# Kernel tuning notes

Measured on AMD Instinct MI355X. Metric: run time of the kernel, lower is better.

## Reference

```python
import jax, jax.numpy as jnp
import numpy as np

N_NODES = 100000
N_EDGES = 1600000
C_IN, C_HID, C_OUT = 32, 32, 8
N_AGENTS = 1000


def _glorot(key, shape):
    fan_in, fan_out = shape[0], shape[1]
    lim = float(np.sqrt(6.0 / (fan_in + fan_out)))
    return jax.random.uniform(key, shape, jnp.float32, -lim, lim)


def setup_inputs() -> dict:
    key = jax.random.key(0)
    ks = jax.random.split(key, 16)
    x = jax.random.normal(ks[0], (N_NODES, C_IN), jnp.float32)
    edge_index = jax.random.randint(ks[1], (2, N_EDGES), 0, N_NODES, jnp.int64)
    d = {"x": x, "edge_index": edge_index}
    dims = [(C_IN, C_HID), (C_HID, C_HID), (C_HID, C_HID)]
    for i, (di, do) in enumerate(dims, start=1):
        d[f"W_l{i}"] = _glorot(ks[2 * i], (di, do))        # neighbor (aggregated) weight
        d[f"b_l{i}"] = jnp.zeros((do,), jnp.float32)
        d[f"W_r{i}"] = _glorot(ks[2 * i + 1], (di, do))    # root/self weight (no bias)
    d["W_out"] = _glorot(ks[10], (C_HID, C_OUT))
    d["b_out"] = jnp.zeros((C_OUT,), jnp.float32)
    return d


def _sage_conv(x, src, dst, W_l, b_l, W_r):
    # mean-aggregate neighbor features at destination nodes
    msg = x[src]                                               # [E, d] gather
    summed = jax.ops.segment_sum(msg, dst, num_segments=N_NODES)
    cnt = jax.ops.segment_sum(jnp.ones((src.shape[0],), x.dtype), dst,
                              num_segments=N_NODES)
    agg = summed / jnp.maximum(cnt, 1.0)[:, None]              # deg==0 -> 0
    return agg @ W_l + b_l + x @ W_r


def reference(x, edge_index, W_l1, b_l1, W_r1, W_l2, b_l2, W_r2,
              W_l3, b_l3, W_r3, W_out, b_out):
    src, dst = edge_index[0], edge_index[1]
    h = jax.nn.relu(_sage_conv(x, src, dst, W_l1, b_l1, W_r1))
    h = jax.nn.relu(_sage_conv(h, src, dst, W_l2, b_l2, W_r2))
    h = jax.nn.relu(_sage_conv(h, src, dst, W_l3, b_l3, W_r3))
    out = h @ W_out + b_out
    return out[:N_AGENTS]
```

## Files before the change

### kernel.cpp

```cpp
#include <hip/hip_runtime.h>
#include <hip/hip_bf16.h>

#define N_NODES 100000
#define N_EDGES 1600000
#define N_AGENTS 1000

#define NB 782
#define ABLK 512
#define CHUNK (N_EDGES / ABLK)
#define CONV_BLOCKS 3125
#define FLAGS_I4 25024
#define FLAG_BLOCKS 98

typedef short s16x8 __attribute__((ext_vector_type(8)));
typedef float f32x4 __attribute__((ext_vector_type(4)));

__device__ __forceinline__ unsigned short f2bf(float f) {
    unsigned u = __float_as_uint(f);
    u += 0x7fffu + ((u >> 16) & 1u);
    return (unsigned short)(u >> 16);
}
__device__ __forceinline__ float bflo(unsigned u) { return __uint_as_float(u << 16); }
__device__ __forceinline__ float bfhi(unsigned u) { return __uint_as_float(u & 0xffff0000u); }

__global__ __launch_bounds__(256) void hist_prep_kernel(
    const int* __restrict__ dst, int* __restrict__ partialT,
    const float* __restrict__ x, unsigned short* __restrict__ xb,
    const float* __restrict__ Wl1, const float* __restrict__ Wr1,
    const float* __restrict__ Wl2, const float* __restrict__ Wr2,
    const float* __restrict__ Wl3, const float* __restrict__ Wr3,
    unsigned short* __restrict__ Wcat, int* __restrict__ flags)
{
    int b = blockIdx.x;
    if (b < ABLK) {
        __shared__ int hist[NB];
        for (int i = threadIdx.x; i < NB; i += 256) hist[i] = 0;
        __syncthreads();
        int beg = b * CHUNK;
        for (int e = beg + threadIdx.x; e < beg + CHUNK; e += 256)
            atomicAdd(&hist[dst[e] >> 7], 1);
        __syncthreads();
        for (int i = threadIdx.x; i < NB; i += 256) partialT[i * ABLK + b] = hist[i];
    } else if (b < ABLK + CONV_BLOCKS) {
        int i = (b - ABLK) * 256 + threadIdx.x;
        float4 v = ((const float4*)x)[i];
        ((ushort4*)xb)[i] = make_ushort4(f2bf(v.x), f2bf(v.y), f2bf(v.z), f2bf(v.w));
    } else if (b < ABLK + CONV_BLOCKS + 24) {
        int gid = (b - ABLK - CONV_BLOCKS) * 256 + threadIdx.x;
        int L = gid >> 11, idx = gid & 2047;
        int k = idx >> 5, n = idx & 31;
        const float* Wl = (L == 0) ? Wl1 : (L == 1) ? Wl2 : Wl3;
        const float* Wr = (L == 0) ? Wr1 : (L == 1) ? Wr2 : Wr3;
        float v = (k < 32) ? Wl[k * 32 + n] : Wr[(k - 32) * 32 + n];
        Wcat[gid] = f2bf(v);
    } else {
        int gid = (b - ABLK - CONV_BLOCKS - 24) * 256 + threadIdx.x;
        if (gid < FLAGS_I4) ((int4*)flags)[gid] = make_int4(0, 0, 0, 0);
    }
}

__global__ __launch_bounds__(256) void bucket_prefix_kernel(
    const int* __restrict__ partialT, int* __restrict__ baseT, int* __restrict__ tot)
{
    int wave = threadIdx.x >> 6, lane = threadIdx.x & 63;
    int t = blockIdx.x * 4 + wave;
    if (t >= NB) return;
    const int4* p = (const int4*)(partialT + (size_t)t * ABLK);
    int4 u0 = p[lane * 2], u1 = p[lane * 2 + 1];
    int v0 = u0.x, v1 = u0.y, v2 = u0.z, v3 = u0.w;
    int v4 = u1.x, v5 = u1.y, v6 = u1.z, v7 = u1.w;
    int p0 = 0, p1 = v0, p2 = p1 + v1, p3 = p2 + v2;
    int p4 = p3 + v3, p5 = p4 + v4, p6 = p5 + v5, p7 = p6 + v6;
    int s = p7 + v7;
    int x = s;
    #pragma unroll
    for (int off = 1; off < 64; off <<= 1) {
        int y = __shfl_up(x, off);
        if (lane >= off) x += y;
    }
    int excl = x - s;
    int4* q = (int4*)(baseT + (size_t)t * ABLK);
    q[lane * 2]     = make_int4(excl + p0, excl + p1, excl + p2, excl + p3);
    q[lane * 2 + 1] = make_int4(excl + p4, excl + p5, excl + p6, excl + p7);
    if (lane == 63) tot[t] = x;
}

__global__ __launch_bounds__(256) void bucket_scatter_kernel(
    const int* __restrict__ src, const int* __restrict__ dst,
    const int* __restrict__ baseT, const int* __restrict__ tot,
    int* __restrict__ bstart, int* __restrict__ ebuf)
{
    __shared__ int cur[NB];
    __shared__ int tsum[256];
    int b = blockIdx.x, t = threadIdx.x;
    int i0 = t * 4;
    int v0 = (i0     < NB) ? tot[i0]     : 0;
    int v1 = (i0 + 1 < NB) ? tot[i0 + 1] : 0;
    int v2 = (i0 + 2 < NB) ? tot[i0 + 2] : 0;
    int v3 = (i0 + 3 < NB) ? tot[i0 + 3] : 0;
    int p1 = v0, p2 = v0 + v1, p3 = v0 + v1 + v2, s4 = p3 + v3;
    tsum[t] = s4;
    __syncthreads();
    for (int off = 1; off < 256; off <<= 1) {
        int u = (t >= off) ? tsum[t - off] : 0;
        __syncthreads();
        tsum[t] += u;
        __syncthreads();
    }
    int excl = tsum[t] - s4;
    int st0 = excl, st1 = excl + p1, st2 = excl + p2, st3 = excl + p3;
    if (i0     < NB) cur[i0]     = st0 + baseT[(size_t)i0 * ABLK + b];
    if (i0 + 1 < NB) cur[i0 + 1] = st1 + baseT[(size_t)(i0 + 1) * ABLK + b];
    if (i0 + 2 < NB) cur[i0 + 2] = st2 + baseT[(size_t)(i0 + 2) * ABLK + b];
    if (i0 + 3 < NB) cur[i0 + 3] = st3 + baseT[(size_t)(i0 + 3) * ABLK + b];
    if (b == 0) {
        if (i0     < NB) bstart[i0]     = st0;
        if (i0 + 1 < NB) bstart[i0 + 1] = st1;
        if (i0 + 2 < NB) bstart[i0 + 2] = st2;
        if (i0 + 3 < NB) bstart[i0 + 3] = st3;
        if (t == 255)    bstart[NB] = tsum[255];
    }
    __syncthreads();
    int beg = b * CHUNK;
    for (int e = beg + threadIdx.x; e < beg + CHUNK; e += 256) {
        int d = dst[e];
        int slot = atomicAdd(&cur[d >> 7], 1);
        ebuf[slot] = src[e] | ((d & 127) << 17);
    }
}

__global__ __launch_bounds__(256) void bucket_csr_kernel(
    const int* __restrict__ bstart, const int* __restrict__ ebuf,
    int* __restrict__ rowptr, float* __restrict__ inv, int* __restrict__ esrc,
    int* __restrict__ flags)
{
    __shared__ int hist4[512], cur4[512], tmp[256];
    int b = blockIdx.x;
    int t = threadIdx.x;
    int beg = bstart[b], end = bstart[b + 1];
    hist4[t] = 0; hist4[t + 256] = 0;
    __syncthreads();
    for (int i = beg + t; i < end; i += 256) {
        int p = ebuf[i];
        int ln = (p >> 17) & 127;
        int cls = (p & 0x1FFFF) >> 15;
        atomicAdd(&hist4[ln * 4 + cls], 1);
    }
    __syncthreads();
    int c0 = 0, c1 = 0, c2 = 0, c3 = 0, v = 0;
    if (t < 128) {
        c0 = hist4[t * 4 + 0]; c1 = hist4[t * 4 + 1];
        c2 = hist4[t * 4 + 2]; c3 = hist4[t * 4 + 3];
        v = c0 + c1 + c2 + c3;
    }
    tmp[t] = v;
    __syncthreads();
    for (int off = 1; off < 256; off <<= 1) {
        int u = (t >= off) ? tmp[t - off] : 0;
        __syncthreads();
        tmp[t] += u;
        __syncthreads();
    }
    int excl = tmp[t] - v;
    int node = b * 128 + t;
    if (t < 128 && node < N_NODES) {
        int start = beg + excl;
        rowptr[node] = start;
        inv[node] = 1.0f / fmaxf((float)v, 1.0f);
        cur4[t * 4 + 0] = start;
        cur4[t * 4 + 1] = start + c0;
        cur4[t * 4 + 2] = start + c0 + c1;
        cur4[t * 4 + 3] = start + c0 + c1 + c2;
        if (node < N_AGENTS) flags[node] = 1;
    }
    if (b == NB - 1 && t == 0) rowptr[N_NODES] = N_EDGES;
    __syncthreads();
    bool agent_bucket = (b < 8);
    for (int i = beg + t; i < end; i += 256) {
        int p = ebuf[i];
        int ln = (p >> 17) & 127;
        int s = p & 0x1FFFF;
        int slot = atomicAdd(&cur4[ln * 4 + (s >> 15)], 1);
        esrc[slot] = s;
        if (agent_bucket && (b * 128 + ln) < N_AGENTS)
            flags[s] = 1;
    }
}

__global__ __launch_bounds__(256) void sage_fused_kernel(
    const int* __restrict__ rowptr, const int* __restrict__ esrc,
    const float* __restrict__ inv, const unsigned short* __restrict__ hb,
    const unsigned short* __restrict__ Wcat, const float* __restrict__ bl,
    const float* __restrict__ Wout, const float* __restrict__ bout,
    void* __restrict__ outp, int n_nodes, int final)
{
    __shared__ unsigned short sW[2048];
    __shared__ float sb[32];
    __shared__ unsigned short smean[64 * 40];
    __shared__ float sh3[64 * 33];
    __shared__ float sWo[256];
    __shared__ float sbo[8];

    int tid = threadIdx.x;
    ((uint4*)sW)[tid] = ((const uint4*)Wcat)[tid];
    if (tid < 32) sb[tid] = bl[tid];
    if (final) {
        sWo[tid] = Wout[tid];
        if (tid < 8) sbo[tid] = bout[tid];
    }

    int lane = tid & 63, wave = tid >> 6;

    int g = lane >> 2, q = lane & 3;
    int nodeA = blockIdx.x * 64 + wave * 16 + g;
    int beg = 0, end = 0;
    if (nodeA < n_nodes) { beg = rowptr[nodeA]; end = rowptr[nodeA + 1]; }
    float a0 = 0.f, a1 = 0.f, a2 = 0.f, a3 = 0.f;
    float a4 = 0.f, a5 = 0.f, a6 = 0.f, a7 = 0.f;
    int j = beg;
    for (; j + 3 < end; j += 4) {
        int s0 = esrc[j];
        int s1 = esrc[j + 1];
        int s2 = esrc[j + 2];
        int s3 = esrc[j + 3];
        uint4 u0 = *(const uint4*)(hb + s0 * 32 + q * 8);
        uint4 u1 = *(const uint4*)(hb + s1 * 32 + q * 8);
        uint4 u2 = *(const uint4*)(hb + s2 * 32 + q * 8);
        uint4 u3 = *(const uint4*)(hb + s3 * 32 + q * 8);
        a0 += bflo(u0.x); a1 += bfhi(u0.x);
        a2 += bflo(u0.y); a3 += bfhi(u0.y);
        a4 += bflo(u0.z); a5 += bfhi(u0.z);
        a6 += bflo(u0.w); a7 += bfhi(u0.w);
        a0 += bflo(u1.x); a1 += bfhi(u1.x);
        a2 += bflo(u1.y); a3 += bfhi(u1.y);
        a4 += bflo(u1.z); a5 += bfhi(u1.z);
        a6 += bflo(u1.w); a7 += bfhi(u1.w);
        a0 += bflo(u2.x); a1 += bfhi(u2.x);
        a2 += bflo(u2.y); a3 += bfhi(u2.y);
        a4 += bflo(u2.z); a5 += bfhi(u2.z);
        a6 += bflo(u2.w); a7 += bfhi(u2.w);
        a0 += bflo(u3.x); a1 += bfhi(u3.x);
        a2 += bflo(u3.y); a3 += bfhi(u3.y);
        a4 += bflo(u3.z); a5 += bfhi(u3.z);
        a6 += bflo(u3.w); a7 += bfhi(u3.w);
    }
    for (; j < end; j++) {
        int s = esrc[j];
        uint4 u = *(const uint4*)(hb + s * 32 + q * 8);
        a0 += bflo(u.x); a1 += bfhi(u.x);
        a2 += bflo(u.y); a3 += bfhi(u.y);
        a4 += bflo(u.z); a5 += bfhi(u.z);
        a6 += bflo(u.w); a7 += bfhi(u.w);
    }
    float iv = (nodeA < n_nodes) ? inv[nodeA] : 0.f;
    uint4 o;
    o.x = (unsigned)f2bf(a0 * iv) | ((unsigned)f2bf(a1 * iv) << 16);
    o.y = (unsigned)f2bf(a2 * iv) | ((unsigned)f2bf(a3 * iv) << 16);
    o.z = (unsigned)f2bf(a4 * iv) | ((unsigned)f2bf(a5 * iv) << 16);
    o.w = (unsigned)f2bf(a6 * iv) | ((unsigned)f2bf(a7 * iv) << 16);
    int mrow = wave * 16 + g;
    *(uint4*)&smean[mrow * 40 + q * 8] = o;
    __syncthreads();

    int l15 = lane & 15, quad = lane >> 4;
    s16x8 bf_[2][2];
    #pragma unroll
    for (int kt = 0; kt < 2; kt++)
        #pragma unroll
        for (int nt = 0; nt < 2; nt++)
            #pragma unroll
            for (int jj = 0; jj < 8; jj++) {
                int k = kt * 32 + quad * 8 + jj;
                bf_[kt][nt][jj] = (short)sW[k * 32 + l15 + nt * 16];
            }
    float bias0 = sb[l15], bias1 = sb[l15 + 16];

    int tilebase = blockIdx.x * 64 + wave * 16;
    int nodeD = tilebase + l15;
    int na = min(nodeD, n_nodes - 1);
    s16x8 am = *(const s16x8*)&smean[(wave * 16 + l15) * 40 + quad * 8];
    s16x8 as = *(const s16x8*)(hb + (size_t)na * 32 + quad * 8);
    f32x4 acc0 = {0.f, 0.f, 0.f, 0.f};
    f32x4 acc1 = {0.f, 0.f, 0.f, 0.f};
    acc0 = __builtin_amdgcn_mfma_f32_16x16x32_bf16(am, bf_[0][0], acc0, 0, 0, 0);
    acc0 = __builtin_amdgcn_mfma_f32_16x16x32_bf16(as, bf_[1][0], acc0, 0, 0, 0);
    acc1 = __builtin_amdgcn_mfma_f32_16x16x32_bf16(am, bf_[0][1], acc1, 0, 0, 0);
    acc1 = __builtin_amdgcn_mfma_f32_16x16x32_bf16(as, bf_[1][1], acc1, 0, 0, 0);

    if (!final) {
        #pragma unroll
        for (int r = 0; r < 4; r++) {
            int onode = tilebase + quad * 4 + r;
            if (onode < n_nodes) {
                ((unsigned short*)outp)[onode * 32 + l15]      = f2bf(fmaxf(acc0[r] + bias0, 0.f));
                ((unsigned short*)outp)[onode * 32 + l15 + 16] = f2bf(fmaxf(acc1[r] + bias1, 0.f));
            }
        }
    } else {
        #pragma unroll
        for (int r = 0; r < 4; r++) {
            int row = wave * 16 + quad * 4 + r;
            sh3[row * 33 + l15]      = fmaxf(acc0[r] + bias0, 0.f);
            sh3[row * 33 + l15 + 16] = fmaxf(acc1[r] + bias1, 0.f);
        }
        __syncthreads();
        #pragma unroll
        for (int i = tid; i < 512; i += 256) {
            int ln = i >> 3, c = i & 7;
            int gn = blockIdx.x * 64 + ln;
            if (gn < N_AGENTS) {
                float ov = sbo[c];
                #pragma unroll
                for (int k = 0; k < 32; k++) ov += sh3[ln * 33 + k] * sWo[k * 8 + c];
                ((float*)outp)[gn * 8 + c] = ov;
            }
        }
    }
}

__global__ __launch_bounds__(256) void sage_fused_flag_kernel(
    const int* __restrict__ rowptr, const int* __restrict__ esrc,
    const float* __restrict__ inv, const unsigned short* __restrict__ hb,
    const unsigned short* __restrict__ Wcat, const float* __restrict__ bl,
    unsigned short* __restrict__ outp, const int* __restrict__ flags,
    int n_nodes)
{
    __shared__ unsigned short sW[2048];
    __shared__ float sb[32];
    __shared__ unsigned short smean[64 * 40];
    __shared__ int sflag[64];

    int tid = threadIdx.x;
    ((uint4*)sW)[tid] = ((const uint4*)Wcat)[tid];
    if (tid < 32) sb[tid] = bl[tid];
    if (tid < 64) {
        int gid = blockIdx.x * 64 + tid;
        sflag[tid] = (gid < n_nodes) ? flags[gid] : 0;
    }
    __syncthreads();

    int lane = tid & 63, wave = tid >> 6;

    int g = lane >> 2, q = lane & 3;
    int lnode = wave * 16 + g;
    int nodeA = blockIdx.x * 64 + lnode;
    int beg = 0, end = 0;
    if (sflag[lnode]) { beg = rowptr[nodeA]; end = rowptr[nodeA + 1]; }
    float a0 = 0.f, a1 = 0.f, a2 = 0.f, a3 = 0.f;
    float a4 = 0.f, a5 = 0.f, a6 = 0.f, a7 = 0.f;
    int j = beg;
    for (; j + 3 < end; j += 4) {
        int s0 = esrc[j];
        int s1 = esrc[j + 1];
        int s2 = esrc[j + 2];
        int s3 = esrc[j + 3];
        uint4 u0 = *(const uint4*)(hb + s0 * 32 + q * 8);
        uint4 u1 = *(const uint4*)(hb + s1 * 32 + q * 8);
        uint4 u2 = *(const uint4*)(hb + s2 * 32 + q * 8);
        uint4 u3 = *(const uint4*)(hb + s3 * 32 + q * 8);
        a0 += bflo(u0.x); a1 += bfhi(u0.x);
        a2 += bflo(u0.y); a3 += bfhi(u0.y);
        a4 += bflo(u0.z); a5 += bfhi(u0.z);
        a6 += bflo(u0.w); a7 += bfhi(u0.w);
        a0 += bflo(u1.x); a1 += bfhi(u1.x);
        a2 += bflo(u1.y); a3 += bfhi(u1.y);
        a4 += bflo(u1.z); a5 += bfhi(u1.z);
        a6 += bflo(u1.w); a7 += bfhi(u1.w);
        a0 += bflo(u2.x); a1 += bfhi(u2.x);
        a2 += bflo(u2.y); a3 += bfhi(u2.y);
        a4 += bflo(u2.z); a5 += bfhi(u2.z);
        a6 += bflo(u2.w); a7 += bfhi(u2.w);
        a0 += bflo(u3.x); a1 += bfhi(u3.x);
        a2 += bflo(u3.y); a3 += bfhi(u3.y);
        a4 += bflo(u3.z); a5 += bfhi(u3.z);
        a6 += bflo(u3.w); a7 += bfhi(u3.w);
    }
    for (; j < end; j++) {
        int s = esrc[j];
        uint4 u = *(const uint4*)(hb + s * 32 + q * 8);
        a0 += bflo(u.x); a1 += bfhi(u.x);
        a2 += bflo(u.y); a3 += bfhi(u.y);
        a4 += bflo(u.z); a5 += bfhi(u.z);
        a6 += bflo(u.w); a7 += bfhi(u.w);
    }
    float iv = sflag[lnode] ? inv[nodeA] : 0.f;
    uint4 o;
    o.x = (unsigned)f2bf(a0 * iv) | ((unsigned)f2bf(a1 * iv) << 16);
    o.y = (unsigned)f2bf(a2 * iv) | ((unsigned)f2bf(a3 * iv) << 16);
    o.z = (unsigned)f2bf(a4 * iv) | ((unsigned)f2bf(a5 * iv) << 16);
    o.w = (unsigned)f2bf(a6 * iv) | ((unsigned)f2bf(a7 * iv) << 16);
    *(uint4*)&smean[lnode * 40 + q * 8] = o;
    __syncthreads();

    int l15 = lane & 15, quad = lane >> 4;
    s16x8 bf_[2][2];
    #pragma unroll
    for (int kt = 0; kt < 2; kt++)
        #pragma unroll
        for (int nt = 0; nt < 2; nt++)
            #pragma unroll
            for (int jj = 0; jj < 8; jj++) {
                int k = kt * 32 + quad * 8 + jj;
                bf_[kt][nt][jj] = (short)sW[k * 32 + l15 + nt * 16];
            }
    float bias0 = sb[l15], bias1 = sb[l15 + 16];

    int tilebase = blockIdx.x * 64 + wave * 16;
    int nodeD = tilebase + l15;
    int na = min(nodeD, n_nodes - 1);
    s16x8 am = *(const s16x8*)&smean[(wave * 16 + l15) * 40 + quad * 8];
    s16x8 as = *(const s16x8*)(hb + (size_t)na * 32 + quad * 8);
    f32x4 acc0 = {0.f, 0.f, 0.f, 0.f};
    f32x4 acc1 = {0.f, 0.f, 0.f, 0.f};
    acc0 = __builtin_amdgcn_mfma_f32_16x16x32_bf16(am, bf_[0][0], acc0, 0, 0, 0);
    acc0 = __builtin_amdgcn_mfma_f32_16x16x32_bf16(as, bf_[1][0], acc0, 0, 0, 0);
    acc1 = __builtin_amdgcn_mfma_f32_16x16x32_bf16(am, bf_[0][1], acc1, 0, 0, 0);
    acc1 = __builtin_amdgcn_mfma_f32_16x16x32_bf16(as, bf_[1][1], acc1, 0, 0, 0);

    #pragma unroll
    for (int r = 0; r < 4; r++) {
        int lr = wave * 16 + quad * 4 + r;
        int onode = tilebase + quad * 4 + r;
        if (onode < n_nodes && sflag[lr]) {
            outp[onode * 32 + l15]      = f2bf(fmaxf(acc0[r] + bias0, 0.f));
            outp[onode * 32 + l15 + 16] = f2bf(fmaxf(acc1[r] + bias1, 0.f));
        }
    }
}

extern "C" void kernel_launch(void* const* d_in, const int* in_sizes, int n_in,
                              void* d_out, int out_size, void* d_ws, size_t ws_size,
                              hipStream_t stream) {
    const float* x   = (const float*)d_in[0];
    const int* ei    = (const int*)d_in[1];
    const float* Wl1 = (const float*)d_in[2];
    const float* bl1 = (const float*)d_in[3];
    const float* Wr1 = (const float*)d_in[4];
    const float* Wl2 = (const float*)d_in[5];
    const float* bl2 = (const float*)d_in[6];
    const float* Wr2 = (const float*)d_in[7];
    const float* Wl3 = (const float*)d_in[8];
    const float* bl3 = (const float*)d_in[9];
    const float* Wr3 = (const float*)d_in[10];
    const float* Wout = (const float*)d_in[11];
    const float* bout = (const float*)d_in[12];
    float* out = (float*)d_out;

    const int* src = ei;
    const int* dst = ei + N_EDGES;

    char* ws = (char*)d_ws;
    int*   rowptr   = (int*)ws;                                ws += (size_t)(N_NODES + 8) * 4;
    float* inv      = (float*)ws;                              ws += (size_t)N_NODES * 4;
    int*   partialT = (int*)ws;                                ws += (size_t)NB * ABLK * 4;
    int*   baseT    = (int*)ws;                                ws += (size_t)NB * ABLK * 4;
    int*   tot      = (int*)ws;                                ws += 784 * 4;
    int*   bstart   = (int*)ws;                                ws += 784 * 4;
    int*   esrc     = (int*)ws;                                ws += (size_t)N_EDGES * 4;
    unsigned short* hXb   = (unsigned short*)ws;               ws += (size_t)N_NODES * 32 * 2;
    unsigned short* hAb   = (unsigned short*)ws;               ws += (size_t)N_NODES * 32 * 2;
    unsigned short* hBb   = (unsigned short*)ws;               ws += (size_t)N_NODES * 32 * 2;
    unsigned short* Wcat  = (unsigned short*)ws;               ws += 3 * 2048 * 2;
    int*   flags    = (int*)ws;                                ws += (size_t)100096 * 4;
    int*   ebuf     = (int*)hAb;

    hist_prep_kernel<<<ABLK + CONV_BLOCKS + 24 + FLAG_BLOCKS, 256, 0, stream>>>(
        dst, partialT, x, hXb, Wl1, Wr1, Wl2, Wr2, Wl3, Wr3, Wcat, flags);
    bucket_prefix_kernel<<<(NB + 3) / 4, 256, 0, stream>>>(partialT, baseT, tot);
    bucket_scatter_kernel<<<ABLK, 256, 0, stream>>>(src, dst, baseT, tot, bstart, ebuf);
    bucket_csr_kernel<<<NB, 256, 0, stream>>>(bstart, ebuf, rowptr, inv, esrc, flags);

    sage_fused_kernel<<<(N_NODES + 63) / 64, 256, 0, stream>>>(
        rowptr, esrc, inv, hXb, Wcat, bl1, Wout, bout, hAb, N_NODES, 0);
    sage_fused_flag_kernel<<<(N_NODES + 63) / 64, 256, 0, stream>>>(
        rowptr, esrc, inv, hAb, Wcat + 2048, bl2, hBb, flags, N_NODES);
    sage_fused_kernel<<<(N_AGENTS + 63) / 64, 256, 0, stream>>>(
        rowptr, esrc, inv, hBb, Wcat + 4096, bl3, Wout, bout, out, N_AGENTS, 1);
}
```

Baseline: 185.1 us.

## Replace two-pass bucket sort CSR build with global atomic node histogram and scatter

The CSR construction no longer uses the partial-histogram/bucket-scatter/bucket-CSR pipeline. It now counts per-(node, src-class) edges with global atomics, scans them per bucket, and scatters edges directly with global atomics into the final slots. This removes the intermediate ebuf pass and the per-block partial tables. Row start and degree are packed into one word, and the inverse degree is computed on the fly instead of loaded. In exchange it depends on heavily contended global atomics over 400K counters, and it caps degree at 2047 and begin offsets at 21 bits.

```diff
diff --git a/kernel.cpp b/kernel.cpp
--- a/kernel.cpp
+++ b/kernel.cpp
@@ -6,11 +6,14 @@
 #define N_AGENTS 1000
 
 #define NB 782
-#define ABLK 512
-#define CHUNK (N_EDGES / ABLK)
 #define CONV_BLOCKS 3125
+#define WCAT_BLOCKS 24
 #define FLAGS_I4 25024
 #define FLAG_BLOCKS 98
+#define NCLS_I4 100096
+#define NCLS_BLOCKS 391
+#define HIST_BLOCKS 1024
+#define SCAT_BLOCKS 2048
 
 typedef short s16x8 __attribute__((ext_vector_type(8)));
 typedef float f32x4 __attribute__((ext_vector_type(4)));
@@ -23,76 +26,63 @@
 __device__ __forceinline__ float bflo(unsigned u) { return __uint_as_float(u << 16); }
 __device__ __forceinline__ float bfhi(unsigned u) { return __uint_as_float(u & 0xffff0000u); }
 
-__global__ __launch_bounds__(256) void hist_prep_kernel(
-    const int* __restrict__ dst, int* __restrict__ partialT,
+__global__ __launch_bounds__(256) void prep_kernel(
     const float* __restrict__ x, unsigned short* __restrict__ xb,
     const float* __restrict__ Wl1, const float* __restrict__ Wr1,
     const float* __restrict__ Wl2, const float* __restrict__ Wr2,
     const float* __restrict__ Wl3, const float* __restrict__ Wr3,
-    unsigned short* __restrict__ Wcat, int* __restrict__ flags)
+    unsigned short* __restrict__ Wcat, int* __restrict__ flags,
+    int* __restrict__ nodecls, int* __restrict__ tot)
 {
     int b = blockIdx.x;
-    if (b < ABLK) {
-        __shared__ int hist[NB];
-        for (int i = threadIdx.x; i < NB; i += 256) hist[i] = 0;
-        __syncthreads();
-        int beg = b * CHUNK;
-        for (int e = beg + threadIdx.x; e < beg + CHUNK; e += 256)
-            atomicAdd(&hist[dst[e] >> 7], 1);
-        __syncthreads();
-        for (int i = threadIdx.x; i < NB; i += 256) partialT[i * ABLK + b] = hist[i];
-    } else if (b < ABLK + CONV_BLOCKS) {
-        int i = (b - ABLK) * 256 + threadIdx.x;
+    if (b < CONV_BLOCKS) {
+        int i = b * 256 + threadIdx.x;
         float4 v = ((const float4*)x)[i];
         ((ushort4*)xb)[i] = make_ushort4(f2bf(v.x), f2bf(v.y), f2bf(v.z), f2bf(v.w));
-    } else if (b < ABLK + CONV_BLOCKS + 24) {
-        int gid = (b - ABLK - CONV_BLOCKS) * 256 + threadIdx.x;
+    } else if (b < CONV_BLOCKS + WCAT_BLOCKS) {
+        int gid = (b - CONV_BLOCKS) * 256 + threadIdx.x;
         int L = gid >> 11, idx = gid & 2047;
         int k = idx >> 5, n = idx & 31;
         const float* Wl = (L == 0) ? Wl1 : (L == 1) ? Wl2 : Wl3;
         const float* Wr = (L == 0) ? Wr1 : (L == 1) ? Wr2 : Wr3;
         float v = (k < 32) ? Wl[k * 32 + n] : Wr[(k - 32) * 32 + n];
         Wcat[gid] = f2bf(v);
+    } else if (b < CONV_BLOCKS + WCAT_BLOCKS + FLAG_BLOCKS) {
+        int gid = (b - CONV_BLOCKS - WCAT_BLOCKS) * 256 + threadIdx.x;
+        if (gid < FLAGS_I4) ((int4*)flags)[gid] = make_int4(0, 0, 0, 0);
+    } else if (b < CONV_BLOCKS + WCAT_BLOCKS + FLAG_BLOCKS + NCLS_BLOCKS) {
+        int gid = (b - CONV_BLOCKS - WCAT_BLOCKS - FLAG_BLOCKS) * 256 + threadIdx.x;
+        ((int4*)nodecls)[gid] = make_int4(0, 0, 0, 0);
     } else {
-        int gid = (b - ABLK - CONV_BLOCKS - 24) * 256 + threadIdx.x;
-        if (gid < FLAGS_I4) ((int4*)flags)[gid] = make_int4(0, 0, 0, 0);
-    }
-}
-
-__global__ __launch_bounds__(256) void bucket_prefix_kernel(
-    const int* __restrict__ partialT, int* __restrict__ baseT, int* __restrict__ tot)
-{
-    int wave = threadIdx.x >> 6, lane = threadIdx.x & 63;
-    int t = blockIdx.x * 4 + wave;
-    if (t >= NB) return;
-    const int4* p = (const int4*)(partialT + (size_t)t * ABLK);
-    int4 u0 = p[lane * 2], u1 = p[lane * 2 + 1];
-    int v0 = u0.x, v1 = u0.y, v2 = u0.z, v3 = u0.w;
-    int v4 = u1.x, v5 = u1.y, v6 = u1.z, v7 = u1.w;
-    int p0 = 0, p1 = v0, p2 = p1 + v1, p3 = p2 + v2;
-    int p4 = p3 + v3, p5 = p4 + v4, p6 = p5 + v5, p7 = p6 + v6;
-    int s = p7 + v7;
-    int x = s;
-    #pragma unroll
-    for (int off = 1; off < 64; off <<= 1) {
-        int y = __shfl_up(x, off);
-        if (lane >= off) x += y;
-    }
-    int excl = x - s;
-    int4* q = (int4*)(baseT + (size_t)t * ABLK);
-    q[lane * 2]     = make_int4(excl + p0, excl + p1, excl + p2, excl + p3);
-    q[lane * 2 + 1] = make_int4(excl + p4, excl + p5, excl + p6, excl + p7);
-    if (lane == 63) tot[t] = x;
-}
-
-__global__ __launch_bounds__(256) void bucket_scatter_kernel(
+        for (int i = threadIdx.x; i < 800; i += 256) tot[i] = 0;
+    }
+}
+
+__global__ __launch_bounds__(256) void hist_kernel(
     const int* __restrict__ src, const int* __restrict__ dst,
-    const int* __restrict__ baseT, const int* __restrict__ tot,
-    int* __restrict__ bstart, int* __restrict__ ebuf)
-{
-    __shared__ int cur[NB];
-    __shared__ int tsum[256];
+    int* __restrict__ nodecls, int* __restrict__ tot)
+{
+    __shared__ int h[NB];
+    for (int i = threadIdx.x; i < NB; i += 256) h[i] = 0;
+    __syncthreads();
+    for (int e = blockIdx.x * 256 + threadIdx.x; e < N_EDGES; e += HIST_BLOCKS * 256) {
+        int d = dst[e], s = src[e];
+        atomicAdd(&nodecls[(d << 2) | (s >> 15)], 1);
+        atomicAdd(&h[d >> 7], 1);
+    }
+    __syncthreads();
+    for (int i = threadIdx.x; i < NB; i += 256)
+        if (h[i]) atomicAdd(&tot[i], h[i]);
+}
+
+__global__ __launch_bounds__(256) void nodescan_kernel(
+    const int* __restrict__ tot, int* __restrict__ cur4,
+    unsigned* __restrict__ pk, int* __restrict__ flags)
+{
+    __shared__ int tsum[256], incl[256], sS[256];
+    __shared__ int sbase;
     int b = blockIdx.x, t = threadIdx.x;
+
     int i0 = t * 4;
     int v0 = (i0     < NB) ? tot[i0]     : 0;
     int v1 = (i0 + 1 < NB) ? tot[i0 + 1] : 0;
@@ -107,89 +97,53 @@
         tsum[t] += u;
         __syncthreads();
     }
-    int excl = tsum[t] - s4;
-    int st0 = excl, st1 = excl + p1, st2 = excl + p2, st3 = excl + p3;
-    if (i0     < NB) cur[i0]     = st0 + baseT[(size_t)i0 * ABLK + b];
-    if (i0 + 1 < NB) cur[i0 + 1] = st1 + baseT[(size_t)(i0 + 1) * ABLK + b];
-    if (i0 + 2 < NB) cur[i0 + 2] = st2 + baseT[(size_t)(i0 + 2) * ABLK + b];
-    if (i0 + 3 < NB) cur[i0 + 3] = st3 + baseT[(size_t)(i0 + 3) * ABLK + b];
-    if (b == 0) {
-        if (i0     < NB) bstart[i0]     = st0;
-        if (i0 + 1 < NB) bstart[i0 + 1] = st1;
-        if (i0 + 2 < NB) bstart[i0 + 2] = st2;
-        if (i0 + 3 < NB) bstart[i0 + 3] = st3;
-        if (t == 255)    bstart[NB] = tsum[255];
-    }
-    __syncthreads();
-    int beg = b * CHUNK;
-    for (int e = beg + threadIdx.x; e < beg + CHUNK; e += 256) {
-        int d = dst[e];
-        int slot = atomicAdd(&cur[d >> 7], 1);
-        ebuf[slot] = src[e] | ((d & 127) << 17);
-    }
-}
-
-__global__ __launch_bounds__(256) void bucket_csr_kernel(
-    const int* __restrict__ bstart, const int* __restrict__ ebuf,
-    int* __restrict__ rowptr, float* __restrict__ inv, int* __restrict__ esrc,
-    int* __restrict__ flags)
-{
-    __shared__ int hist4[512], cur4[512], tmp[256];
-    int b = blockIdx.x;
-    int t = threadIdx.x;
-    int beg = bstart[b], end = bstart[b + 1];
-    hist4[t] = 0; hist4[t + 256] = 0;
-    __syncthreads();
-    for (int i = beg + t; i < end; i += 256) {
-        int p = ebuf[i];
-        int ln = (p >> 17) & 127;
-        int cls = (p & 0x1FFFF) >> 15;
-        atomicAdd(&hist4[ln * 4 + cls], 1);
-    }
-    __syncthreads();
-    int c0 = 0, c1 = 0, c2 = 0, c3 = 0, v = 0;
+    if ((b >> 2) == t) {
+        int excl = tsum[t] - s4;
+        int o = b & 3;
+        sbase = excl + (o == 0 ? 0 : o == 1 ? p1 : o == 2 ? p2 : p3);
+    }
+    __syncthreads();
+    int base = sbase;
+
+    int2 ab = ((const int2*)(cur4 + (size_t)b * 512))[t];
+    int a = ab.x, c = ab.y;
+    int s2 = a + c;
+    incl[t] = s2; sS[t] = s2;
+    __syncthreads();
+    for (int off = 1; off < 256; off <<= 1) {
+        int u = (t >= off) ? incl[t - off] : 0;
+        __syncthreads();
+        incl[t] += u;
+        __syncthreads();
+    }
+    int eprev = incl[t] - s2;
+    ((int2*)(cur4 + (size_t)b * 512))[t] = make_int2(base + eprev, base + eprev + a);
+    __syncthreads();
     if (t < 128) {
-        c0 = hist4[t * 4 + 0]; c1 = hist4[t * 4 + 1];
-        c2 = hist4[t * 4 + 2]; c3 = hist4[t * 4 + 3];
-        v = c0 + c1 + c2 + c3;
-    }
-    tmp[t] = v;
-    __syncthreads();
-    for (int off = 1; off < 256; off <<= 1) {
-        int u = (t >= off) ? tmp[t - off] : 0;
-        __syncthreads();
-        tmp[t] += u;
-        __syncthreads();
-    }
-    int excl = tmp[t] - v;
-    int node = b * 128 + t;
-    if (t < 128 && node < N_NODES) {
-        int start = beg + excl;
-        rowptr[node] = start;
-        inv[node] = 1.0f / fmaxf((float)v, 1.0f);
-        cur4[t * 4 + 0] = start;
-        cur4[t * 4 + 1] = start + c0;
-        cur4[t * 4 + 2] = start + c0 + c1;
-        cur4[t * 4 + 3] = start + c0 + c1 + c2;
+        int e0 = incl[2 * t] - sS[2 * t];
+        int cnt = incl[2 * t + 1] - e0;
+        unsigned beg = (unsigned)(base + e0);
+        int node = b * 128 + t;
+        pk[node] = (beg << 11) | (unsigned)min(cnt, 2047);
         if (node < N_AGENTS) flags[node] = 1;
     }
-    if (b == NB - 1 && t == 0) rowptr[N_NODES] = N_EDGES;
-    __syncthreads();
-    bool agent_bucket = (b < 8);
-    for (int i = beg + t; i < end; i += 256) {
-        int p = ebuf[i];
-        int ln = (p >> 17) & 127;
-        int s = p & 0x1FFFF;
-        int slot = atomicAdd(&cur4[ln * 4 + (s >> 15)], 1);
+}
+
+__global__ __launch_bounds__(256) void scatter_kernel(
+    const int* __restrict__ src, const int* __restrict__ dst,
+    int* __restrict__ cur4, int* __restrict__ esrc, int* __restrict__ flags)
+{
+    for (int e = blockIdx.x * 256 + threadIdx.x; e < N_EDGES; e += SCAT_BLOCKS * 256) {
+        int d = dst[e], s = src[e];
+        int slot = atomicAdd(&cur4[(d << 2) | (s >> 15)], 1);
         esrc[slot] = s;
-        if (agent_bucket && (b * 128 + ln) < N_AGENTS)
-            flags[s] = 1;
+        if (d < N_AGENTS) flags[s] = 1;
     }
 }
 
 __global__ __launch_bounds__(256) void sage_fused_kernel(
-    const int* __restrict__ rowptr, const int* __restrict__ esrc,
-    const float* __restrict__ inv, const unsigned short* __restrict__ hb,
+    const unsigned* __restrict__ pk, const int* __restrict__ esrc,
+    const unsigned short* __restrict__ hb,
     const unsigned short* __restrict__ Wcat, const float* __restrict__ bl,
     const float* __restrict__ Wout, const float* __restrict__ bout,
     void* __restrict__ outp, int n_nodes, int final)
@@ -213,8 +167,13 @@
 
     int g = lane >> 2, q = lane & 3;
     int nodeA = blockIdx.x * 64 + wave * 16 + g;
-    int beg = 0, end = 0;
-    if (nodeA < n_nodes) { beg = rowptr[nodeA]; end = rowptr[nodeA + 1]; }
+    int beg = 0, cnt = 0;
+    if (nodeA < n_nodes) {
+        unsigned pkv = pk[nodeA];
+        beg = (int)(pkv >> 11);
+        cnt = (int)(pkv & 2047u);
+    }
+    int end = beg + cnt;
     float a0 = 0.f, a1 = 0.f, a2 = 0.f, a3 = 0.f;
     float a4 = 0.f, a5 = 0.f, a6 = 0.f, a7 = 0.f;
     int j = beg;
@@ -252,7 +211,7 @@
         a4 += bflo(u.z); a5 += bfhi(u.z);
         a6 += bflo(u.w); a7 += bfhi(u.w);
     }
-    float iv = (nodeA < n_nodes) ? inv[nodeA] : 0.f;
+    float iv = 1.0f / fmaxf((float)cnt, 1.0f);
     uint4 o;
     o.x = (unsigned)f2bf(a0 * iv) | ((unsigned)f2bf(a1 * iv) << 16);
     o.y = (unsigned)f2bf(a2 * iv) | ((unsigned)f2bf(a3 * iv) << 16);
@@ -319,8 +278,8 @@
 }
 
 __global__ __launch_bounds__(256) void sage_fused_flag_kernel(
-    const int* __restrict__ rowptr, const int* __restrict__ esrc,
-    const float* __restrict__ inv, const unsigned short* __restrict__ hb,
+    const unsigned* __restrict__ pk, const int* __restrict__ esrc,
+    const unsigned short* __restrict__ hb,
     const unsigned short* __restrict__ Wcat, const float* __restrict__ bl,
     unsigned short* __restrict__ outp, const int* __restrict__ flags,
     int n_nodes)
@@ -344,8 +303,13 @@
     int g = lane >> 2, q = lane & 3;
     int lnode = wave * 16 + g;
     int nodeA = blockIdx.x * 64 + lnode;
-    int beg = 0, end = 0;
-    if (sflag[lnode]) { beg = rowptr[nodeA]; end = rowptr[nodeA + 1]; }
+    int beg = 0, cnt = 0;
+    if (sflag[lnode]) {
+        unsigned pkv = pk[nodeA];
+        beg = (int)(pkv >> 11);
+        cnt = (int)(pkv & 2047u);
+    }
+    int end = beg + cnt;
     float a0 = 0.f, a1 = 0.f, a2 = 0.f, a3 = 0.f;
     float a4 = 0.f, a5 = 0.f, a6 = 0.f, a7 = 0.f;
     int j = beg;
@@ -383,7 +347,7 @@
         a4 += bflo(u.z); a5 += bfhi(u.z);
         a6 += bflo(u.w); a7 += bfhi(u.w);
     }
-    float iv = sflag[lnode] ? inv[nodeA] : 0.f;
+    float iv = 1.0f / fmaxf((float)cnt, 1.0f);
     uint4 o;
     o.x = (unsigned)f2bf(a0 * iv) | ((unsigned)f2bf(a1 * iv) << 16);
     o.y = (unsigned)f2bf(a2 * iv) | ((unsigned)f2bf(a3 * iv) << 16);
@@ -450,30 +414,26 @@
     const int* dst = ei + N_EDGES;
 
     char* ws = (char*)d_ws;
-    int*   rowptr   = (int*)ws;                                ws += (size_t)(N_NODES + 8) * 4;
-    float* inv      = (float*)ws;                              ws += (size_t)N_NODES * 4;
-    int*   partialT = (int*)ws;                                ws += (size_t)NB * ABLK * 4;
-    int*   baseT    = (int*)ws;                                ws += (size_t)NB * ABLK * 4;
-    int*   tot      = (int*)ws;                                ws += 784 * 4;
-    int*   bstart   = (int*)ws;                                ws += 784 * 4;
-    int*   esrc     = (int*)ws;                                ws += (size_t)N_EDGES * 4;
-    unsigned short* hXb   = (unsigned short*)ws;               ws += (size_t)N_NODES * 32 * 2;
-    unsigned short* hAb   = (unsigned short*)ws;               ws += (size_t)N_NODES * 32 * 2;
-    unsigned short* hBb   = (unsigned short*)ws;               ws += (size_t)N_NODES * 32 * 2;
-    unsigned short* Wcat  = (unsigned short*)ws;               ws += 3 * 2048 * 2;
-    int*   flags    = (int*)ws;                                ws += (size_t)100096 * 4;
-    int*   ebuf     = (int*)hAb;
-
-    hist_prep_kernel<<<ABLK + CONV_BLOCKS + 24 + FLAG_BLOCKS, 256, 0, stream>>>(
-        dst, partialT, x, hXb, Wl1, Wr1, Wl2, Wr2, Wl3, Wr3, Wcat, flags);
-    bucket_prefix_kernel<<<(NB + 3) / 4, 256, 0, stream>>>(partialT, baseT, tot);
-    bucket_scatter_kernel<<<ABLK, 256, 0, stream>>>(src, dst, baseT, tot, bstart, ebuf);
-    bucket_csr_kernel<<<NB, 256, 0, stream>>>(bstart, ebuf, rowptr, inv, esrc, flags);
+    int*      nodecls = (int*)ws;                              ws += (size_t)NB * 512 * 4;
+    int*      tot     = (int*)ws;                              ws += 800 * 4;
+    unsigned* pk      = (unsigned*)ws;                         ws += (size_t)100096 * 4;
+    int*      esrc    = (int*)ws;                              ws += (size_t)N_EDGES * 4;
+    unsigned short* hXb  = (unsigned short*)ws;                ws += (size_t)N_NODES * 32 * 2;
+    unsigned short* hAb  = (unsigned short*)ws;                ws += (size_t)N_NODES * 32 * 2;
+    unsigned short* hBb  = (unsigned short*)ws;                ws += (size_t)N_NODES * 32 * 2;
+    unsigned short* Wcat = (unsigned short*)ws;                ws += 3 * 2048 * 2;
+    int*      flags   = (int*)ws;                              ws += (size_t)100096 * 4;
+
+    prep_kernel<<<CONV_BLOCKS + WCAT_BLOCKS + FLAG_BLOCKS + NCLS_BLOCKS + 1, 256, 0, stream>>>(
+        x, hXb, Wl1, Wr1, Wl2, Wr2, Wl3, Wr3, Wcat, flags, nodecls, tot);
+    hist_kernel<<<HIST_BLOCKS, 256, 0, stream>>>(src, dst, nodecls, tot);
+    nodescan_kernel<<<NB, 256, 0, stream>>>(tot, nodecls, pk, flags);
+    scatter_kernel<<<SCAT_BLOCKS, 256, 0, stream>>>(src, dst, nodecls, esrc, flags);
 
     sage_fused_kernel<<<(N_NODES + 63) / 64, 256, 0, stream>>>(
-        rowptr, esrc, inv, hXb, Wcat, bl1, Wout, bout, hAb, N_NODES, 0);
+        pk, esrc, hXb, Wcat, bl1, Wout, bout, hAb, N_NODES, 0);
     sage_fused_flag_kernel<<<(N_NODES + 63) / 64, 256, 0, stream>>>(
-        rowptr, esrc, inv, hAb, Wcat + 2048, bl2, hBb, flags, N_NODES);
+        pk, esrc, hAb, Wcat + 2048, bl2, hBb, flags, N_NODES);
     sage_fused_kernel<<<(N_AGENTS + 63) / 64, 256, 0, stream>>>(
-        rowptr, esrc, inv, hBb, Wcat + 4096, bl3, Wout, bout, out, N_AGENTS, 1);
-}
+        pk, esrc, hBb, Wcat + 4096, bl3, Wout, bout, out, N_AGENTS, 1);
+}
```

Measured after the change: 350.2 us. 89.2% more time.
